# Kernel optimization log

Hardware: AMD Instinct MI355X
Metric: run time of the kernel (lower is better)

The kernel has to match this reference:

```python
import jax, jax.numpy as jnp
import numpy as np

K = 3            # kernel_size
PAD = K // 2
E = K * K        # num_elements

def setup_inputs() -> dict:
    key = jax.random.key(0)
    k1, k2, k3 = jax.random.split(key, 3)
    B, H, W, C = 8, 224, 224, 32
    inp = jax.random.uniform(k1, (B, H, W, C), dtype=jnp.float32)
    kernel = 0.5 + 0.05 * jax.random.uniform(k2, (E, 1, 1, 1, C), dtype=jnp.float32)
    mask = 0.75 + 0.05 * jax.random.uniform(k3, (E, 1, 1, 1, C), dtype=jnp.float32)
    return {"inp": inp, "kernel": kernel, "mask": mask}

def _shifted_stack(inp):
    # Replicates the TF loop ordering: element 0 is the unshifted input (center
    # tap), then taps in (y, x) raster order skipping the center.
    B, H, W, C = inp.shape
    padded = jnp.pad(inp, ((0, 0), (PAD, PAD), (PAD, PAD), (0, 0)))
    taps = [inp]
    for y in range(K):
        for x in range(K):
            if y != PAD or x != PAD:
                taps.append(padded[:, y:y + H, x:x + W, :])
    return jnp.stack(taps, axis=0)  # [E, B, H, W, C]

def reference(inp, kernel, mask):
    shifted = _shifted_stack(inp)                                   # [E,B,H,W,C]
    m = jnp.abs(mask) / (jnp.max(jnp.abs(mask)) + 1e-6)             # [E,1,1,1,C]
    sm = shifted * m                                                # masked taps
    diff = sm - kernel
    abs_diff = jnp.abs(diff)
    norm_1 = jnp.sum(abs_diff, axis=0)                              # [B,H,W,C]
    mean_diff = jnp.mean(diff, axis=0)                              # [B,H,W,C]
    variation_diff = jnp.sum(jnp.abs(abs_diff - mean_diff), axis=0) # [B,H,W,C]
    return (1.0 - variation_diff / E) * (1.0 - norm_1 / E)
```

## Files before the change

### kernel.cpp

```cpp
#include <hip/hip_runtime.h>

#define E  9
#define B_ 8
#define H_ 224
#define W_ 224
#define C_ 32
#define TH 7
#define WT 8
#define STRIPS (H_ / TH)
#define WTILES (W_ / WT)
#define NBLK (B_ * STRIPS * WTILES)

__global__ __launch_bounds__(256) void fm_main(const float* __restrict__ inp,
                                               const float* __restrict__ kern,
                                               const float* __restrict__ mask,
                                               float* __restrict__ out) {
    int t = threadIdx.x;

    int bid = blockIdx.x;
    int swz = (bid & 7) * (NBLK / 8) + (bid >> 3);
    int bw  = swz % WTILES;
    int t2  = swz / WTILES;
    int hs  = (t2 % STRIPS) * TH;
    int b   = t2 / STRIPS;

    int c  = t & 31;
    int wl = t >> 5;
    int w  = bw * WT + wl;

    float cm[E], ck[E];
    float mx = 0.f;
#pragma unroll
    for (int e = 0; e < E; ++e) {
        float mv = fabsf(mask[e * C_ + c]);
        ck[e] = kern[e * C_ + c];
        mx = fmaxf(mx, mv);
        cm[e] = mv;
    }
    mx = fmaxf(mx, __shfl_xor(mx, 1));
    mx = fmaxf(mx, __shfl_xor(mx, 2));
    mx = fmaxf(mx, __shfl_xor(mx, 4));
    mx = fmaxf(mx, __shfl_xor(mx, 8));
    mx = fmaxf(mx, __shfl_xor(mx, 16));
    float inv = 1.f / (mx + 1e-6f);
#pragma unroll
    for (int e = 0; e < E; ++e) cm[e] *= inv;
#pragma unroll
    for (int e = 0; e < E; ++e)
        asm volatile("" : "+v"(cm[e]), "+v"(ck[e]));

    const float* base = inp + (((size_t)b * H_ * W_ + w) * C_) + c;
    bool wm = (w > 0);
    bool wp = (w < W_ - 1);

    float win[3][3];

    auto ld3 = [&](int hh, float* r) {
        if ((unsigned)hh < (unsigned)H_) {
            const float* p = base + (size_t)hh * (W_ * C_);
            r[0] = wm ? p[-C_] : 0.f;
            r[1] = p[0];
            r[2] = wp ? p[C_] : 0.f;
        } else {
            r[0] = 0.f; r[1] = 0.f; r[2] = 0.f;
        }
    };

    ld3(hs - 1, win[0]);
    ld3(hs,     win[1]);

    const float inv9 = 1.f / 9.f;

#pragma unroll
    for (int s = 0; s < TH; ++s) {
        ld3(hs + s + 1, win[(s + 2) % 3]);

        const float* rm1 = win[(s + 0) % 3];
        const float* r0  = win[(s + 1) % 3];
        const float* rp1 = win[(s + 2) % 3];

        float taps[E] = { r0[1],
                          rm1[0], rm1[1], rm1[2],
                          r0[0],          r0[2],
                          rp1[0], rp1[1], rp1[2] };

        float d[E];
        float n = 0.f, sm = 0.f;
#pragma unroll
        for (int e = 0; e < E; ++e) {
            float dd = fmaf(taps[e], cm[e], -ck[e]);
            d[e] = dd;
            n  += fabsf(dd);
            sm += dd;
        }
        float nm = sm * (-inv9);
        float v = 0.f;
#pragma unroll
        for (int e = 0; e < E; ++e)
            v += fabsf(fabsf(d[e]) + nm);

        float o = fmaf(v, -inv9, 1.f) * fmaf(n, -inv9, 1.f);

        float* op = out + (((size_t)b * H_ + (hs + s)) * W_ + w) * C_ + c;
        __builtin_nontemporal_store(o, op);
    }
}

extern "C" void kernel_launch(void* const* d_in, const int* in_sizes, int n_in,
                              void* d_out, int out_size, void* d_ws, size_t ws_size,
                              hipStream_t stream) {
    const float* inp  = (const float*)d_in[0];
    const float* kern = (const float*)d_in[1];
    const float* mask = (const float*)d_in[2];
    float* out = (float*)d_out;

    fm_main<<<NBLK, 256, 0, stream>>>(inp, kern, mask, out);
}
```

Measured before the change: 30.31 us.

## Issue all input row loads up front and restructure tap loop for ILP

Loads all TH+2 input rows (27 values) into registers before reading the mask and kernel, so every global load is in flight at once instead of being streamed one row per output step. The compute loop is reordered to iterate over taps outermost and output rows innermost, with per-tap mask and kernel values computed on the fly. It also pins occupancy with amdgpu_waves_per_eu(4,4). Holding all the differences as a [9][7] register array raises register pressure considerably, and the fixed waves-per-eu hint limits how many waves can hide latency.

```diff
diff --git a/kernel.cpp b/kernel.cpp
--- a/kernel.cpp
+++ b/kernel.cpp
@@ -11,10 +11,12 @@
 #define WTILES (W_ / WT)
 #define NBLK (B_ * STRIPS * WTILES)
 
-__global__ __launch_bounds__(256) void fm_main(const float* __restrict__ inp,
-                                               const float* __restrict__ kern,
-                                               const float* __restrict__ mask,
-                                               float* __restrict__ out) {
+__global__ __launch_bounds__(256)
+__attribute__((amdgpu_waves_per_eu(4, 4)))
+void fm_main(const float* __restrict__ inp,
+             const float* __restrict__ kern,
+             const float* __restrict__ mask,
+             float* __restrict__ out) {
     int t = threadIdx.x;
 
     int bid = blockIdx.x;
@@ -28,14 +30,30 @@
     int wl = t >> 5;
     int w  = bw * WT + wl;
 
-    float cm[E], ck[E];
+    const float* base = inp + (((size_t)b * H_ * W_ + w) * C_) + c;
+    bool wm = (w > 0);
+    bool wp = (w < W_ - 1);
+
+    float tap[TH + 2][3];
+#pragma unroll
+    for (int r = 0; r < TH + 2; ++r) {
+        int hh = hs - 1 + r;
+        if ((unsigned)hh < (unsigned)H_) {
+            const float* p = base + (size_t)hh * (W_ * C_);
+            tap[r][0] = wm ? p[-C_] : 0.f;
+            tap[r][1] = p[0];
+            tap[r][2] = wp ? p[C_] : 0.f;
+        } else {
+            tap[r][0] = 0.f; tap[r][1] = 0.f; tap[r][2] = 0.f;
+        }
+    }
+
+    float mv[E];
     float mx = 0.f;
 #pragma unroll
     for (int e = 0; e < E; ++e) {
-        float mv = fabsf(mask[e * C_ + c]);
-        ck[e] = kern[e * C_ + c];
-        mx = fmaxf(mx, mv);
-        cm[e] = mv;
+        mv[e] = fabsf(mask[e * C_ + c]);
+        mx = fmaxf(mx, mv[e]);
     }
     mx = fmaxf(mx, __shfl_xor(mx, 1));
     mx = fmaxf(mx, __shfl_xor(mx, 2));
@@ -43,63 +61,38 @@
     mx = fmaxf(mx, __shfl_xor(mx, 8));
     mx = fmaxf(mx, __shfl_xor(mx, 16));
     float inv = 1.f / (mx + 1e-6f);
-#pragma unroll
-    for (int e = 0; e < E; ++e) cm[e] *= inv;
-#pragma unroll
-    for (int e = 0; e < E; ++e)
-        asm volatile("" : "+v"(cm[e]), "+v"(ck[e]));
 
-    const float* base = inp + (((size_t)b * H_ * W_ + w) * C_) + c;
-    bool wm = (w > 0);
-    bool wp = (w < W_ - 1);
-
-    float win[3][3];
-
-    auto ld3 = [&](int hh, float* r) {
-        if ((unsigned)hh < (unsigned)H_) {
-            const float* p = base + (size_t)hh * (W_ * C_);
-            r[0] = wm ? p[-C_] : 0.f;
-            r[1] = p[0];
-            r[2] = wp ? p[C_] : 0.f;
-        } else {
-            r[0] = 0.f; r[1] = 0.f; r[2] = 0.f;
-        }
-    };
-
-    ld3(hs - 1, win[0]);
-    ld3(hs,     win[1]);
+    const int dyA[E] = {0, -1, -1, -1, 0, 0, 1, 1, 1};
+    const int dxA[E] = {0, -1,  0,  1, -1, 1, -1, 0, 1};
 
     const float inv9 = 1.f / 9.f;
 
+    float n[TH], sm[TH], dd[E][TH];
+#pragma unroll
+    for (int s = 0; s < TH; ++s) { n[s] = 0.f; sm[s] = 0.f; }
+
+#pragma unroll
+    for (int e = 0; e < E; ++e) {
+        float m = mv[e] * inv;
+        float k = kern[e * C_ + c];
+#pragma unroll
+        for (int s = 0; s < TH; ++s) {
+            float d0 = fmaf(tap[s + 1 + dyA[e]][1 + dxA[e]], m, -k);
+            dd[e][s] = d0;
+            n[s]  += fabsf(d0);
+            sm[s] += d0;
+        }
+    }
+
 #pragma unroll
     for (int s = 0; s < TH; ++s) {
-        ld3(hs + s + 1, win[(s + 2) % 3]);
-
-        const float* rm1 = win[(s + 0) % 3];
-        const float* r0  = win[(s + 1) % 3];
-        const float* rp1 = win[(s + 2) % 3];
-
-        float taps[E] = { r0[1],
-                          rm1[0], rm1[1], rm1[2],
-                          r0[0],          r0[2],
-                          rp1[0], rp1[1], rp1[2] };
-
-        float d[E];
-        float n = 0.f, sm = 0.f;
-#pragma unroll
-        for (int e = 0; e < E; ++e) {
-            float dd = fmaf(taps[e], cm[e], -ck[e]);
-            d[e] = dd;
-            n  += fabsf(dd);
-            sm += dd;
-        }
-        float nm = sm * (-inv9);
+        float nm = sm[s] * (-inv9);
         float v = 0.f;
 #pragma unroll
         for (int e = 0; e < E; ++e)
-            v += fabsf(fabsf(d[e]) + nm);
+            v += fabsf(fabsf(dd[e][s]) + nm);
 
-        float o = fmaf(v, -inv9, 1.f) * fmaf(n, -inv9, 1.f);
+        float o = fmaf(v, -inv9, 1.f) * fmaf(n[s], -inv9, 1.f);
 
         float* op = out + (((size_t)b * H_ + (hs + s)) * W_ + w) * C_ + c;
         __builtin_nontemporal_store(o, op);
```

Result: faster. 27.56 us (-9.1%).
